# Kernel optimization log

Hardware: AMD Instinct MI355X
Metric: run time of the kernel (lower is better)

The kernel has to match this reference:

```python
import jax, jax.numpy as jnp
import numpy as np

B, S, D, H = 4, 1024, 512, 8
DH = D // H
NEG = -1e32


def setup_inputs() -> dict:
    key = jax.random.key(0)
    ks = jax.random.split(key, 8)
    w_scale = (6.0 / (D + D)) ** 0.5  # xavier_uniform bound scale (approx, gaussian draw)
    def nrm(i, shape, scale=1.0):
        return jax.random.normal(ks[i], shape, jnp.float32) * scale
    return {
        "q": nrm(0, (B, S, D)),
        "k": nrm(1, (B, S, D)),
        "v": nrm(2, (B, S, D)),
        # causal lower-triangular mask (attend to self and past)
        "mask": jnp.tril(jnp.ones((1, 1, S, S), jnp.int32)),
        "Wq": nrm(3, (D, D), w_scale), "bq": jnp.zeros((D,), jnp.float32),
        "Wk": nrm(4, (D, D), w_scale), "bk": jnp.zeros((D,), jnp.float32),
        "Wv": nrm(5, (D, D), w_scale), "bv": jnp.zeros((D,), jnp.float32),
        "Wo": nrm(6, (D, D), w_scale), "bo": jnp.zeros((D,), jnp.float32),
        "gammas": nrm(7, (H, 1, 1), 0.5),
    }


def reference(q, k, v, mask, Wq, bq, Wk, bk, Wv, bv, Wo, bo, gammas):
    maskf = mask.astype(jnp.float32)
    neg = mask == 0

    def proj(x, W, b):
        # nn.Linear: x @ W.T + b, then split heads -> [B,H,S,DH]
        return (x @ W.T + b).reshape(B, S, H, DH).transpose(0, 2, 1, 3)

    qh, kh, vh = proj(q, Wq, bq), proj(k, Wk, bk), proj(v, Wv, bv)
    scores = jnp.einsum('bhqd,bhkd->bhqk', qh, kh) / jnp.sqrt(jnp.float32(DH))

    pos = jnp.arange(S, dtype=jnp.float32)
    position_effect = jnp.abs(pos[None, :] - pos[:, None])  # [S,S] = |i - j|

    # no-grad branch: masked softmax -> cumulative / total attention mass
    sm = jax.nn.softmax(jnp.where(neg, NEG, scores), axis=-1) * maskf
    distcum = jnp.cumsum(sm, axis=-1)
    disttotal = jnp.sum(sm, axis=-1, keepdims=True)
    dist_scores = jnp.sqrt(jnp.maximum((disttotal - distcum) * position_effect, 0.0))
    dist_scores = jax.lax.stop_gradient(dist_scores)

    gamma = -jax.nn.softplus(gammas)[None]  # [1,H,1,1], learned decay rate
    total_effect = jnp.clip(jnp.exp(dist_scores * gamma), 1e-5, 1e5)

    attn = jax.nn.softmax(jnp.where(neg, NEG, scores * total_effect), axis=-1)
    attn = attn.at[:, :, 0, :].set(0.0)  # zero_pad=True: zero out first query row
    # dropout is identity at eval time

    out = jnp.einsum('bhqk,bhkd->bhqd', attn, vh)
    concat = out.transpose(0, 2, 1, 3).reshape(B, S, D)
    output = concat @ Wo.T + bo
    return output, attn
```

## Files before the change

kernel.cpp:

```cpp
#include <hip/hip_runtime.h>
#include <hip/hip_bf16.h>

typedef __attribute__((ext_vector_type(8))) _Float16 half8;
typedef __attribute__((ext_vector_type(4))) _Float16 half4v;
typedef __attribute__((ext_vector_type(4))) float f32x4;

#define MFMA16(a, b, c) __builtin_amdgcn_mfma_f32_16x16x32_f16((a), (b), (c), 0, 0, 0)

static constexpr int Bb = 4, Ss = 1024, Dd = 512, Hh = 8, DHh = 64;
static constexpr float LOG2E = 1.44269504f;
static constexpr float FNEG = -65504.f;

__device__ __forceinline__ half4v f2h4(float4 f) {
  half4v h;
  h[0] = (_Float16)f.x; h[1] = (_Float16)f.y;
  h[2] = (_Float16)f.z; h[3] = (_Float16)f.w;
  return h;
}

template<int MODE>
__global__ __launch_bounds__(256) void gemm_k(
    const void* A0v, const void* A1v, const float* Bm0, const float* Bm1,
    const float* bias0, const float* bias1, void* C0v, void* C1v,
    int M, int N, int K)
{
  __shared__ _Float16 As[128 * 72];
  __shared__ _Float16 Bs[64 * 72];

  const int tid = threadIdx.x;
  const int w = tid >> 6, l = tid & 63;
  const int wr = w >> 1, wc = w & 1;
  const int l4 = l >> 4, lm = l & 15;
  const int m0 = blockIdx.x * 128, n0 = blockIdx.y * 64;
  const int z = (MODE == 0) ? (int)blockIdx.z : 0;

  const float* Af = (const float*)(z ? A1v : A0v);
  const ushort* Ab = (const ushort*)A0v;
  const float* Bw = z ? Bm1 : Bm0;
  const float* bias = z ? bias1 : bias0;

  f32x4 zz = {0.f, 0.f, 0.f, 0.f};
  f32x4 acc[4][2];
#pragma unroll
  for (int i2 = 0; i2 < 4; ++i2)
#pragma unroll
    for (int j = 0; j < 2; ++j) acc[i2][j] = zz;

  for (int k0 = 0; k0 < K; k0 += 64) {
#pragma unroll
    for (int it = 0; it < 8; ++it) {
      int f4 = it * 256 + tid;
      int rowi = f4 >> 4, c4 = (f4 & 15) << 2;
      if constexpr (MODE == 1) {
        ushort4 u = *(const ushort4*)&Ab[(size_t)(m0 + rowi) * K + k0 + c4];
        *(ushort4*)&As[rowi * 72 + c4] = u;
      } else {
        float4 f = *(const float4*)&Af[(size_t)(m0 + rowi) * K + k0 + c4];
        *(half4v*)&As[rowi * 72 + c4] = f2h4(f);
      }
    }
#pragma unroll
    for (int it = 0; it < 4; ++it) {
      int f4 = it * 256 + tid;
      int rowi = f4 >> 4, c4 = (f4 & 15) << 2;
      float4 f = *(const float4*)&Bw[(size_t)(n0 + rowi) * K + k0 + c4];
      *(half4v*)&Bs[rowi * 72 + c4] = f2h4(f);
    }
    __syncthreads();
#pragma unroll
    for (int ks = 0; ks < 2; ++ks) {
      half8 a[4], b[2];
#pragma unroll
      for (int mf = 0; mf < 4; ++mf)
        a[mf] = *(const half8*)&As[(wr * 64 + mf * 16 + lm) * 72 + ks * 32 + l4 * 8];
#pragma unroll
      for (int nf = 0; nf < 2; ++nf)
        b[nf] = *(const half8*)&Bs[(wc * 32 + nf * 16 + lm) * 72 + ks * 32 + l4 * 8];
#pragma unroll
      for (int mf = 0; mf < 4; ++mf)
#pragma unroll
        for (int nf = 0; nf < 2; ++nf)
          acc[mf][nf] = MFMA16(a[mf], b[nf], acc[mf][nf]);
    }
    __syncthreads();
  }

  _Float16* Ch = (_Float16*)(z ? C1v : C0v);
  float* Cf = (float*)C0v;
#pragma unroll
  for (int mf = 0; mf < 4; ++mf) {
#pragma unroll
    for (int nf = 0; nf < 2; ++nf) {
      int row0 = m0 + wr * 64 + mf * 16 + l4 * 4;
      int col = n0 + wc * 32 + nf * 16 + lm;
      f32x4 vv = acc[mf][nf];
#pragma unroll
      for (int r = 0; r < 4; ++r) {
        int row = row0 + r;
        float val = vv[r];
        if constexpr (MODE == 0) {
          val += bias[col];
          int idx = (((row >> 10) * Hh + (col >> 6)) * Ss + (row & 1023)) * DHh + (col & 63);
          Ch[idx] = (_Float16)val;
        } else if constexpr (MODE == 2) {
          val += bias[row];
          int idx = (((col >> 10) * Hh + (row >> 6)) * DHh + (row & 63)) * Ss + (col & 1023);
          Ch[idx] = (_Float16)val;
        } else {
          val += bias[col];
          Cf[(size_t)row * N + col] = val;
        }
      }
    }
  }
}

__global__ __launch_bounds__(512, 4) void attn_k(
    const _Float16* __restrict__ qh, const _Float16* __restrict__ kh,
    const _Float16* __restrict__ vT, const float* __restrict__ gammas,
    float* __restrict__ attn_out, _Float16* __restrict__ concat)
{
  constexpr int TW = 1048;
  __shared__ __align__(16) float smemf[(32 * TW * 2 + 1024) / 4];
  _Float16* tile = (_Float16*)smemf;
  float* pmax = smemf + (32 * TW * 2) / 4;

  const int tid = threadIdx.x;
  const int w = tid >> 6, l = tid & 63;
  const int l4 = l >> 4, lm = l & 15;
  const int bh = blockIdx.y;
  const int b = bh >> 3, h = bh & 7;

  const float g = gammas[h];
  const float g2 = -log1pf(__expf(g)) * LOG2E;

  f32x4 zz = {0.f, 0.f, 0.f, 0.f};
  constexpr float SC2 = 0.125f * LOG2E;

  for (int half = 0; half < 2; ++half) {
    const int qr0 = half ? (Ss - 32 - blockIdx.x * 32) : (blockIdx.x * 32);
    const int nvalid = qr0 + 32;
    __syncthreads();

    const _Float16* Qp = qh + ((size_t)bh * Ss + qr0) * DHh;
    const _Float16* Kp = kh + (size_t)bh * Ss * DHh;

    {
      const int NF = nvalid >> 4;
      const int NFpad = ((nvalid + 63) & ~63) >> 4;
      half8 aq[2][2];
#pragma unroll
      for (int mf = 0; mf < 2; ++mf)
#pragma unroll
        for (int ks = 0; ks < 2; ++ks)
          aq[mf][ks] = *(const half8*)&Qp[(mf * 16 + lm) * DHh + ks * 32 + l4 * 8];

      float pmr[2][4];
#pragma unroll
      for (int mf = 0; mf < 2; ++mf)
#pragma unroll
        for (int r = 0; r < 4; ++r) pmr[mf][r] = -3.0e38f;

      for (int f = w; f < NFpad; f += 8) {
        f32x4 acc[2] = {zz, zz};
        const bool live = (f < NF);
        if (live) {
#pragma unroll
          for (int ks = 0; ks < 2; ++ks) {
            half8 bb = *(const half8*)&Kp[(size_t)(f * 16 + lm) * DHh + ks * 32 + l4 * 8];
            acc[0] = MFMA16(aq[0][ks], bb, acc[0]);
            acc[1] = MFMA16(aq[1][ks], bb, acc[1]);
          }
        }
        const int colc = f * 16 + lm;
#pragma unroll
        for (int mf = 0; mf < 2; ++mf)
#pragma unroll
          for (int r = 0; r < 4; ++r) {
            const int rg = mf * 16 + l4 * 4 + r;
            float val = (live && colc <= qr0 + rg) ? acc[mf][r] * SC2 : FNEG;
            tile[rg * TW + colc] = (_Float16)val;
            pmr[mf][r] = fmaxf(pmr[mf][r], val);
          }
      }
#pragma unroll
      for (int d = 1; d < 16; d <<= 1)
#pragma unroll
        for (int mf = 0; mf < 2; ++mf)
#pragma unroll
          for (int r = 0; r < 4; ++r)
            pmr[mf][r] = fmaxf(pmr[mf][r], __shfl_xor(pmr[mf][r], d, 16));
      if (lm == 0) {
#pragma unroll
        for (int mf = 0; mf < 2; ++mf)
#pragma unroll
          for (int r = 0; r < 4; ++r)
            pmax[(mf * 16 + l4 * 4 + r) * 8 + w] = pmr[mf][r];
      }
    }
    __syncthreads();

    {
      const int r = tid >> 4, t = tid & 15;
      const int i = qr0 + r;
      const int L = i + 1;
      const int nch = (L + 63) >> 6;
      _Float16* row = tile + r * TW;

      float mx = (t < 8) ? pmax[r * 8 + t] : -3.0e38f;
#pragma unroll
      for (int d = 8; d; d >>= 1) mx = fmaxf(mx, __shfl_xor(mx, d, 16));

      float T = 0.f;
      for (int c = 0; c < nch; ++c) {
        half4v s4 = *(const half4v*)&row[(c << 6) + (t << 2)];
#pragma unroll
        for (int j = 0; j < 4; ++j) T += exp2f((float)s4[j] - mx);
      }
#pragma unroll
      for (int d = 8; d; d >>= 1) T += __shfl_xor(T, d, 16);
      const float invT = 1.f / T;

      float carry = 0.f, m2 = -3.0e38f;
      for (int c = 0; c < nch; ++c) {
        const int col = (c << 6) + (t << 2);
        half4v s4 = *(const half4v*)&row[col];
        float s[4], e[4];
#pragma unroll
        for (int j = 0; j < 4; ++j) {
          s[j] = (float)s4[j];
          e[j] = exp2f(s[j] - mx);
        }
        const float lsum = (e[0] + e[1]) + (e[2] + e[3]);
        float sc = lsum;
#pragma unroll
        for (int d = 1; d < 16; d <<= 1) {
          float o = __shfl_up(sc, d, 16);
          if (t >= d) sc += o;
        }
        float run = carry + (sc - lsum);
        carry += __shfl(sc, 15, 16);
        const float dj = (float)(i - col);
        half4v o4;
#pragma unroll
        for (int j = 0; j < 4; ++j) {
          run += e[j];
          float prod = fmaxf((T - run) * invT * (dj - (float)j), 0.f);
          float dist = sqrtf(prod);
          float eff = fmaxf(exp2f(g2 * dist), 1e-5f);
          float l2 = s[j] * eff;
          o4[j] = (_Float16)l2;
          m2 = fmaxf(m2, l2);
        }
        *(half4v*)&row[col] = o4;
      }
#pragma unroll
      for (int d = 8; d; d >>= 1) m2 = fmaxf(m2, __shfl_xor(m2, d, 16));

      float Z2 = 0.f;
      for (int c = 0; c < nch; ++c) {
        const int col = (c << 6) + (t << 2);
        half4v l4v = *(const half4v*)&row[col];
        half4v u4;
#pragma unroll
        for (int j = 0; j < 4; ++j) {
          float u = exp2f((float)l4v[j] - m2);
          Z2 += u;
          u4[j] = (_Float16)u;
        }
        *(half4v*)&row[col] = u4;
      }
#pragma unroll
      for (int d = 8; d; d >>= 1) Z2 += __shfl_xor(Z2, d, 16);
      const float invZ2 = 1.f / Z2;

      const bool zrow = (i == 0);
      float* arow = attn_out + ((size_t)bh * Ss + i) * Ss;
      for (int c = 0; c < Ss / 64; ++c) {
        const int col = (c << 6) + (t << 2);
        float4 pv = {0.f, 0.f, 0.f, 0.f};
        float* pp = (float*)&pv;
        if (c < nch) {
          if (!zrow) {
            half4v u4 = *(const half4v*)&row[col];
#pragma unroll
            for (int j = 0; j < 4; ++j) pp[j] = (float)u4[j] * invZ2;
          }
          half4v p4;
#pragma unroll
          for (int j = 0; j < 4; ++j) p4[j] = (_Float16)pp[j];
          *(half4v*)&row[col] = p4;
        }
        *(float4*)&arow[col] = pv;
      }
    }
    __syncthreads();

    f32x4 acc2[2][4];
#pragma unroll
    for (int mf = 0; mf < 2; ++mf)
#pragma unroll
      for (int nf = 0; nf < 4; ++nf) acc2[mf][nf] = zz;
    {
      const int NC = nvalid >> 5;
      const _Float16* Vp = vT + (size_t)bh * DHh * Ss;
      for (int c = w; c < NC; c += 8) {
        const int kb = c << 5;
        half8 pa[2];
#pragma unroll
        for (int mf = 0; mf < 2; ++mf)
          pa[mf] = *(const half8*)&tile[(mf * 16 + lm) * TW + kb + l4 * 8];
#pragma unroll
        for (int nf = 0; nf < 4; ++nf) {
          half8 bb = *(const half8*)&Vp[(size_t)(nf * 16 + lm) * Ss + kb + l4 * 8];
          acc2[0][nf] = MFMA16(pa[0], bb, acc2[0][nf]);
          acc2[1][nf] = MFMA16(pa[1], bb, acc2[1][nf]);
        }
      }
    }
    __syncthreads();
    float* pps = smemf;
#pragma unroll
    for (int mf = 0; mf < 2; ++mf)
#pragma unroll
      for (int nf = 0; nf < 4; ++nf)
#pragma unroll
        for (int r = 0; r < 4; ++r)
          pps[w * 2048 + (mf * 16 + l4 * 4 + r) * 64 + nf * 16 + lm] = acc2[mf][nf][r];
    __syncthreads();
    for (int idx = tid; idx < 2048; idx += 512) {
      int mr = idx >> 6, nc = idx & 63;
      float ssum = 0.f;
#pragma unroll
      for (int ww = 0; ww < 8; ++ww) ssum += pps[ww * 2048 + idx];
      concat[((size_t)(b * Ss + qr0 + mr)) * Dd + h * DHh + nc] = (_Float16)ssum;
    }
  }
}

extern "C" void kernel_launch(void* const* d_in, const int* in_sizes, int n_in,
                              void* d_out, int out_size, void* d_ws, size_t ws_size,
                              hipStream_t stream) {
  const float* q  = (const float*)d_in[0];
  const float* k  = (const float*)d_in[1];
  const float* v  = (const float*)d_in[2];
  const float* Wq = (const float*)d_in[4];
  const float* bq = (const float*)d_in[5];
  const float* Wk = (const float*)d_in[6];
  const float* bk = (const float*)d_in[7];
  const float* Wv = (const float*)d_in[8];
  const float* bv = (const float*)d_in[9];
  const float* Wo = (const float*)d_in[10];
  const float* bo = (const float*)d_in[11];
  const float* gm = (const float*)d_in[12];

  _Float16* qhb = (_Float16*)d_ws;
  _Float16* khb = qhb + 2097152;
  _Float16* vT  = khb + 2097152;
  _Float16* cc  = vT  + 2097152;

  float* out  = (float*)d_out;
  float* attn = out + (size_t)Bb * Ss * Dd;

  gemm_k<0><<<dim3(32, 8, 2), 256, 0, stream>>>(q, k, Wq, Wk, bq, bk, qhb, khb,
                                                4096, 512, 512);
  gemm_k<2><<<dim3(4, 64, 1), 256, 0, stream>>>(Wv, nullptr, v, nullptr, bv, nullptr,
                                                vT, nullptr, 512, 4096, 512);
  attn_k<<<dim3(16, 32), 512, 0, stream>>>(qhb, khb, vT, gm, attn, cc);
  gemm_k<1><<<dim3(32, 8, 1), 256, 0, stream>>>(cc, nullptr, Wo, nullptr, bo, nullptr,
                                                out, nullptr, 4096, 512, 512);
}
```

Before: 105.9 us.

## Stream attention in 512-column panels with online softmax stats and recomputed QK

Replaces the full-row score tile held in shared memory with 512-column panels. The first pass computes online max and sum statistics, and QK^T is recomputed for a Z2 pass and again for the output pass. The PV product is accumulated per panel, one 16x16 fragment per wave, which removes the cross-wave reduction through shared memory. Shared memory per block shrinks, allowing more blocks per CU (launch bounds 6) and one query tile per block over a doubled grid. The cost is running QK^T and the exp/sqrt effect math three times instead of once, plus a fixed max shift (max(mx,0)) for the second softmax instead of the true row max.

```diff
diff --git a/kernel.cpp b/kernel.cpp
--- a/kernel.cpp
+++ b/kernel.cpp
@@ -115,226 +115,262 @@
   }
 }
 
-__global__ __launch_bounds__(512, 4) void attn_k(
+__global__ __launch_bounds__(512, 6) void attn_k(
     const _Float16* __restrict__ qh, const _Float16* __restrict__ kh,
     const _Float16* __restrict__ vT, const float* __restrict__ gammas,
     float* __restrict__ attn_out, _Float16* __restrict__ concat)
 {
-  constexpr int TW = 1048;
-  __shared__ __align__(16) float smemf[(32 * TW * 2 + 1024) / 4];
-  _Float16* tile = (_Float16*)smemf;
-  float* pmax = smemf + (32 * TW * 2) / 4;
+  constexpr int TW = 528;
+  __shared__ __align__(16) _Float16 tile[32 * TW];
+  __shared__ float pm[256], pt[256];
 
   const int tid = threadIdx.x;
   const int w = tid >> 6, l = tid & 63;
   const int l4 = l >> 4, lm = l & 15;
   const int bh = blockIdx.y;
   const int b = bh >> 3, h = bh & 7;
+  const int qr0 = Ss - 32 - blockIdx.x * 32;
+  const int nvalid = qr0 + 32;
+  const int NF = nvalid >> 4;
+  const int Npan = (nvalid + 511) >> 9;
 
   const float g = gammas[h];
   const float g2 = -log1pf(__expf(g)) * LOG2E;
+  constexpr float SC2 = 0.125f * LOG2E;
+
+  const _Float16* Qp = qh + ((size_t)bh * Ss + qr0) * DHh;
+  const _Float16* Kp = kh + (size_t)bh * Ss * DHh;
+  const _Float16* Vp = vT + (size_t)bh * DHh * Ss;
 
   f32x4 zz = {0.f, 0.f, 0.f, 0.f};
-  constexpr float SC2 = 0.125f * LOG2E;
-
-  for (int half = 0; half < 2; ++half) {
-    const int qr0 = half ? (Ss - 32 - blockIdx.x * 32) : (blockIdx.x * 32);
-    const int nvalid = qr0 + 32;
-    __syncthreads();
-
-    const _Float16* Qp = qh + ((size_t)bh * Ss + qr0) * DHh;
-    const _Float16* Kp = kh + (size_t)bh * Ss * DHh;
-
-    {
-      const int NF = nvalid >> 4;
-      const int NFpad = ((nvalid + 63) & ~63) >> 4;
-      half8 aq[2][2];
+
+  half8 aq[2][2];
+#pragma unroll
+  for (int mf = 0; mf < 2; ++mf)
+#pragma unroll
+    for (int ks = 0; ks < 2; ++ks)
+      aq[mf][ks] = *(const half8*)&Qp[(mf * 16 + lm) * DHh + ks * 32 + l4 * 8];
+
+  {
+    float m_[2][4], t_[2][4];
+#pragma unroll
+    for (int mf = 0; mf < 2; ++mf)
+#pragma unroll
+      for (int r = 0; r < 4; ++r) { m_[mf][r] = -3.0e38f; t_[mf][r] = 0.f; }
+
+    for (int f = w; f < NF; f += 8) {
+      f32x4 acc[2] = {zz, zz};
+      const int colc = f * 16 + lm;
+#pragma unroll
+      for (int ks = 0; ks < 2; ++ks) {
+        half8 bb = *(const half8*)&Kp[(size_t)colc * DHh + ks * 32 + l4 * 8];
+        acc[0] = MFMA16(aq[0][ks], bb, acc[0]);
+        acc[1] = MFMA16(aq[1][ks], bb, acc[1]);
+      }
 #pragma unroll
       for (int mf = 0; mf < 2; ++mf)
 #pragma unroll
-        for (int ks = 0; ks < 2; ++ks)
-          aq[mf][ks] = *(const half8*)&Qp[(mf * 16 + lm) * DHh + ks * 32 + l4 * 8];
-
-      float pmr[2][4];
+        for (int r = 0; r < 4; ++r) {
+          const int rg = mf * 16 + l4 * 4 + r;
+          const bool vld = colc <= qr0 + rg;
+          float s = (float)(_Float16)(acc[mf][r] * SC2);
+          float sv = vld ? s : -3.0e38f;
+          float mN = fmaxf(m_[mf][r], sv);
+          t_[mf][r] = t_[mf][r] * exp2f(m_[mf][r] - mN) + (vld ? exp2f(sv - mN) : 0.f);
+          m_[mf][r] = mN;
+        }
+    }
+#pragma unroll
+    for (int d = 1; d < 16; d <<= 1)
 #pragma unroll
       for (int mf = 0; mf < 2; ++mf)
 #pragma unroll
-        for (int r = 0; r < 4; ++r) pmr[mf][r] = -3.0e38f;
-
-      for (int f = w; f < NFpad; f += 8) {
+        for (int r = 0; r < 4; ++r) {
+          float mo = __shfl_xor(m_[mf][r], d, 16);
+          float to = __shfl_xor(t_[mf][r], d, 16);
+          float mN = fmaxf(m_[mf][r], mo);
+          t_[mf][r] = t_[mf][r] * exp2f(m_[mf][r] - mN) + to * exp2f(mo - mN);
+          m_[mf][r] = mN;
+        }
+    if (lm == 0) {
+#pragma unroll
+      for (int mf = 0; mf < 2; ++mf)
+#pragma unroll
+        for (int r = 0; r < 4; ++r) {
+          const int rg = mf * 16 + l4 * 4 + r;
+          pm[rg * 8 + w] = m_[mf][r];
+          pt[rg * 8 + w] = t_[mf][r];
+        }
+    }
+  }
+  __syncthreads();
+
+  const int rr_ = tid >> 4, t16 = tid & 15;
+  const int i_ = qr0 + rr_;
+
+  float mx = -3.0e38f, T = 0.f;
+#pragma unroll
+  for (int ww = 0; ww < 8; ++ww) {
+    float mo = pm[rr_ * 8 + ww], to = pt[rr_ * 8 + ww];
+    float mN = fmaxf(mx, mo);
+    T = T * exp2f(mx - mN) + to * exp2f(mo - mN);
+    mx = mN;
+  }
+  const float invT = 1.f / T;
+  const float Msh = fmaxf(mx, 0.f);
+
+  float Z2 = 0.f;
+  {
+    float carry = 0.f;
+    for (int p = 0; p < Npan; ++p) {
+#pragma unroll
+      for (int j = 0; j < 4; ++j) {
+        const int floc = w + j * 8;
+        const int f = p * 32 + floc;
+        const int colc = f * 16 + lm;
         f32x4 acc[2] = {zz, zz};
-        const bool live = (f < NF);
-        if (live) {
+        if (f < NF) {
 #pragma unroll
           for (int ks = 0; ks < 2; ++ks) {
-            half8 bb = *(const half8*)&Kp[(size_t)(f * 16 + lm) * DHh + ks * 32 + l4 * 8];
+            half8 bb = *(const half8*)&Kp[(size_t)colc * DHh + ks * 32 + l4 * 8];
             acc[0] = MFMA16(aq[0][ks], bb, acc[0]);
             acc[1] = MFMA16(aq[1][ks], bb, acc[1]);
           }
         }
-        const int colc = f * 16 + lm;
+        const int lcol = floc * 16 + lm;
 #pragma unroll
         for (int mf = 0; mf < 2; ++mf)
 #pragma unroll
           for (int r = 0; r < 4; ++r) {
             const int rg = mf * 16 + l4 * 4 + r;
-            float val = (live && colc <= qr0 + rg) ? acc[mf][r] * SC2 : FNEG;
-            tile[rg * TW + colc] = (_Float16)val;
-            pmr[mf][r] = fmaxf(pmr[mf][r], val);
+            float val = (f < NF && colc <= qr0 + rg) ? acc[mf][r] * SC2 : FNEG;
+            tile[rg * TW + lcol] = (_Float16)val;
           }
       }
-#pragma unroll
-      for (int d = 1; d < 16; d <<= 1)
-#pragma unroll
-        for (int mf = 0; mf < 2; ++mf)
-#pragma unroll
-          for (int r = 0; r < 4; ++r)
-            pmr[mf][r] = fmaxf(pmr[mf][r], __shfl_xor(pmr[mf][r], d, 16));
-      if (lm == 0) {
-#pragma unroll
-        for (int mf = 0; mf < 2; ++mf)
-#pragma unroll
-          for (int r = 0; r < 4; ++r)
-            pmax[(mf * 16 + l4 * 4 + r) * 8 + w] = pmr[mf][r];
-      }
-    }
-    __syncthreads();
-
-    {
-      const int r = tid >> 4, t = tid & 15;
-      const int i = qr0 + r;
-      const int L = i + 1;
-      const int nch = (L + 63) >> 6;
-      _Float16* row = tile + r * TW;
-
-      float mx = (t < 8) ? pmax[r * 8 + t] : -3.0e38f;
-#pragma unroll
-      for (int d = 8; d; d >>= 1) mx = fmaxf(mx, __shfl_xor(mx, d, 16));
-
-      float T = 0.f;
-      for (int c = 0; c < nch; ++c) {
-        half4v s4 = *(const half4v*)&row[(c << 6) + (t << 2)];
-#pragma unroll
-        for (int j = 0; j < 4; ++j) T += exp2f((float)s4[j] - mx);
-      }
-#pragma unroll
-      for (int d = 8; d; d >>= 1) T += __shfl_xor(T, d, 16);
-      const float invT = 1.f / T;
-
-      float carry = 0.f, m2 = -3.0e38f;
-      for (int c = 0; c < nch; ++c) {
-        const int col = (c << 6) + (t << 2);
-        half4v s4 = *(const half4v*)&row[col];
+      __syncthreads();
+      for (int cl = 0; cl < 8; ++cl) {
+        const int cb = p * 512 + cl * 64;
+        if (cb > i_) break;
+        half4v s4 = *(const half4v*)&tile[rr_ * TW + cl * 64 + (t16 << 2)];
         float s[4], e[4];
 #pragma unroll
-        for (int j = 0; j < 4; ++j) {
-          s[j] = (float)s4[j];
-          e[j] = exp2f(s[j] - mx);
-        }
+        for (int j = 0; j < 4; ++j) { s[j] = (float)s4[j]; e[j] = exp2f(s[j] - mx); }
         const float lsum = (e[0] + e[1]) + (e[2] + e[3]);
         float sc = lsum;
 #pragma unroll
         for (int d = 1; d < 16; d <<= 1) {
           float o = __shfl_up(sc, d, 16);
-          if (t >= d) sc += o;
+          if (t16 >= d) sc += o;
         }
         float run = carry + (sc - lsum);
         carry += __shfl(sc, 15, 16);
-        const float dj = (float)(i - col);
-        half4v o4;
+        const float dj = (float)(i_ - (cb + (t16 << 2)));
 #pragma unroll
         for (int j = 0; j < 4; ++j) {
           run += e[j];
           float prod = fmaxf((T - run) * invT * (dj - (float)j), 0.f);
-          float dist = sqrtf(prod);
-          float eff = fmaxf(exp2f(g2 * dist), 1e-5f);
-          float l2 = s[j] * eff;
-          o4[j] = (_Float16)l2;
-          m2 = fmaxf(m2, l2);
-        }
-        *(half4v*)&row[col] = o4;
-      }
-#pragma unroll
-      for (int d = 8; d; d >>= 1) m2 = fmaxf(m2, __shfl_xor(m2, d, 16));
-
-      float Z2 = 0.f;
-      for (int c = 0; c < nch; ++c) {
-        const int col = (c << 6) + (t << 2);
-        half4v l4v = *(const half4v*)&row[col];
-        half4v u4;
+          float eff = fmaxf(exp2f(g2 * sqrtf(prod)), 1e-5f);
+          Z2 += exp2f(s[j] * eff - Msh);
+        }
+      }
+      __syncthreads();
+    }
+  }
+#pragma unroll
+  for (int d = 1; d < 16; d <<= 1) Z2 += __shfl_xor(Z2, d, 16);
+  const float invZ2 = 1.f / Z2;
+
+  f32x4 accO = zz;
+  const int mfw = w >> 2, nfw = w & 3;
+  {
+    float carry = 0.f;
+    const bool zrow = (i_ == 0);
+    float* arow = attn_out + ((size_t)bh * Ss + i_) * Ss;
+    const float4 z4 = {0.f, 0.f, 0.f, 0.f};
+    const half4v hz4 = {(_Float16)0.f, (_Float16)0.f, (_Float16)0.f, (_Float16)0.f};
+
+    for (int p = 0; p < Npan; ++p) {
+#pragma unroll
+      for (int j = 0; j < 4; ++j) {
+        const int floc = w + j * 8;
+        const int f = p * 32 + floc;
+        const int colc = f * 16 + lm;
+        f32x4 acc[2] = {zz, zz};
+        if (f < NF) {
+#pragma unroll
+          for (int ks = 0; ks < 2; ++ks) {
+            half8 bb = *(const half8*)&Kp[(size_t)colc * DHh + ks * 32 + l4 * 8];
+            acc[0] = MFMA16(aq[0][ks], bb, acc[0]);
+            acc[1] = MFMA16(aq[1][ks], bb, acc[1]);
+          }
+        }
+        const int lcol = floc * 16 + lm;
+#pragma unroll
+        for (int mf = 0; mf < 2; ++mf)
+#pragma unroll
+          for (int r = 0; r < 4; ++r) {
+            const int rg = mf * 16 + l4 * 4 + r;
+            float val = (f < NF && colc <= qr0 + rg) ? acc[mf][r] * SC2 : FNEG;
+            tile[rg * TW + lcol] = (_Float16)val;
+          }
+      }
+      __syncthreads();
+      for (int cl = 0; cl < 8; ++cl) {
+        const int cb = p * 512 + cl * 64;
+        const int lofs = rr_ * TW + cl * 64 + (t16 << 2);
+        if (cb > i_) {
+          *(half4v*)&tile[lofs] = hz4;
+          *(float4*)&arow[cb + (t16 << 2)] = z4;
+          continue;
+        }
+        half4v s4 = *(const half4v*)&tile[lofs];
+        float s[4], e[4];
+#pragma unroll
+        for (int j = 0; j < 4; ++j) { s[j] = (float)s4[j]; e[j] = exp2f(s[j] - mx); }
+        const float lsum = (e[0] + e[1]) + (e[2] + e[3]);
+        float sc = lsum;
+#pragma unroll
+        for (int d = 1; d < 16; d <<= 1) {
+          float o = __shfl_up(sc, d, 16);
+          if (t16 >= d) sc += o;
+        }
+        float run = carry + (sc - lsum);
+        carry += __shfl(sc, 15, 16);
+        const float dj = (float)(i_ - (cb + (t16 << 2)));
+        float4 pv = z4;
+        float* pp = (float*)&pv;
+        half4v p4;
 #pragma unroll
         for (int j = 0; j < 4; ++j) {
-          float u = exp2f((float)l4v[j] - m2);
-          Z2 += u;
-          u4[j] = (_Float16)u;
-        }
-        *(half4v*)&row[col] = u4;
-      }
-#pragma unroll
-      for (int d = 8; d; d >>= 1) Z2 += __shfl_xor(Z2, d, 16);
-      const float invZ2 = 1.f / Z2;
-
-      const bool zrow = (i == 0);
-      float* arow = attn_out + ((size_t)bh * Ss + i) * Ss;
-      for (int c = 0; c < Ss / 64; ++c) {
-        const int col = (c << 6) + (t << 2);
-        float4 pv = {0.f, 0.f, 0.f, 0.f};
-        float* pp = (float*)&pv;
-        if (c < nch) {
-          if (!zrow) {
-            half4v u4 = *(const half4v*)&row[col];
-#pragma unroll
-            for (int j = 0; j < 4; ++j) pp[j] = (float)u4[j] * invZ2;
-          }
-          half4v p4;
-#pragma unroll
-          for (int j = 0; j < 4; ++j) p4[j] = (_Float16)pp[j];
-          *(half4v*)&row[col] = p4;
-        }
-        *(float4*)&arow[col] = pv;
-      }
-    }
-    __syncthreads();
-
-    f32x4 acc2[2][4];
-#pragma unroll
-    for (int mf = 0; mf < 2; ++mf)
-#pragma unroll
-      for (int nf = 0; nf < 4; ++nf) acc2[mf][nf] = zz;
-    {
-      const int NC = nvalid >> 5;
-      const _Float16* Vp = vT + (size_t)bh * DHh * Ss;
-      for (int c = w; c < NC; c += 8) {
-        const int kb = c << 5;
-        half8 pa[2];
-#pragma unroll
-        for (int mf = 0; mf < 2; ++mf)
-          pa[mf] = *(const half8*)&tile[(mf * 16 + lm) * TW + kb + l4 * 8];
-#pragma unroll
-        for (int nf = 0; nf < 4; ++nf) {
-          half8 bb = *(const half8*)&Vp[(size_t)(nf * 16 + lm) * Ss + kb + l4 * 8];
-          acc2[0][nf] = MFMA16(pa[0], bb, acc2[0][nf]);
-          acc2[1][nf] = MFMA16(pa[1], bb, acc2[1][nf]);
-        }
-      }
-    }
-    __syncthreads();
-    float* pps = smemf;
-#pragma unroll
-    for (int mf = 0; mf < 2; ++mf)
-#pragma unroll
-      for (int nf = 0; nf < 4; ++nf)
-#pragma unroll
-        for (int r = 0; r < 4; ++r)
-          pps[w * 2048 + (mf * 16 + l4 * 4 + r) * 64 + nf * 16 + lm] = acc2[mf][nf][r];
-    __syncthreads();
-    for (int idx = tid; idx < 2048; idx += 512) {
-      int mr = idx >> 6, nc = idx & 63;
-      float ssum = 0.f;
-#pragma unroll
-      for (int ww = 0; ww < 8; ++ww) ssum += pps[ww * 2048 + idx];
-      concat[((size_t)(b * Ss + qr0 + mr)) * Dd + h * DHh + nc] = (_Float16)ssum;
-    }
+          run += e[j];
+          float prod = fmaxf((T - run) * invT * (dj - (float)j), 0.f);
+          float eff = fmaxf(exp2f(g2 * sqrtf(prod)), 1e-5f);
+          float u = exp2f(s[j] * eff - Msh);
+          float P = zrow ? 0.f : u * invZ2;
+          pp[j] = P;
+          p4[j] = (_Float16)P;
+        }
+        *(half4v*)&tile[lofs] = p4;
+        *(float4*)&arow[cb + (t16 << 2)] = pv;
+      }
+      __syncthreads();
+      const int ksmax = min(16, (nvalid - p * 512 + 31) >> 5);
+      for (int ks = 0; ks < ksmax; ++ks) {
+        const int kb = ks * 32;
+        half8 pa = *(const half8*)&tile[(mfw * 16 + lm) * TW + kb + l4 * 8];
+        half8 bb = *(const half8*)&Vp[(size_t)(nfw * 16 + lm) * Ss + p * 512 + kb + l4 * 8];
+        accO = MFMA16(pa, bb, accO);
+      }
+      __syncthreads();
+    }
+    for (int c = Npan * 8; c < 16; ++c)
+      *(float4*)&arow[c * 64 + (t16 << 2)] = z4;
+  }
+
+#pragma unroll
+  for (int r = 0; r < 4; ++r) {
+    const int row = qr0 + mfw * 16 + l4 * 4 + r;
+    concat[((size_t)(b * Ss + row)) * Dd + h * DHh + nfw * 16 + lm] = (_Float16)accO[r];
   }
 }
 
@@ -366,7 +402,7 @@
                                                 4096, 512, 512);
   gemm_k<2><<<dim3(4, 64, 1), 256, 0, stream>>>(Wv, nullptr, v, nullptr, bv, nullptr,
                                                 vT, nullptr, 512, 4096, 512);
-  attn_k<<<dim3(16, 32), 512, 0, stream>>>(qhb, khb, vT, gm, attn, cc);
+  attn_k<<<dim3(32, 32), 512, 0, stream>>>(qhb, khb, vT, gm, attn, cc);
   gemm_k<1><<<dim3(32, 8, 1), 256, 0, stream>>>(cc, nullptr, Wo, nullptr, bo, nullptr,
                                                 out, nullptr, 4096, 512, 512);
 }
```

Result: slower. 243.3 us (+129.7%).

## Fuse online softmax denominator into QK pass and merge decay/exp passes

Applied to the files above, without the earlier changes.

Computes the running max and exp-sum per row online during the QK^T MFMA pass, so the separate pass that recomputed the first softmax denominator is dropped. The decayed-logit pass and the second exp pass are merged by using a fixed shift max(rowmax, 0) instead of a recomputed second max. The per-wave partial max and sum now live in a padding region of the tile row, which removes the separate pmax array. The fixed shift relies on decay factors at most 1 so that exp2 of the scaled logit stays bounded. It also adds two exp2 per element to the QK loop.

```diff
diff --git a/kernel.cpp b/kernel.cpp
--- a/kernel.cpp
+++ b/kernel.cpp
@@ -120,10 +120,8 @@
     const _Float16* __restrict__ vT, const float* __restrict__ gammas,
     float* __restrict__ attn_out, _Float16* __restrict__ concat)
 {
-  constexpr int TW = 1048;
-  __shared__ __align__(16) float smemf[(32 * TW * 2 + 1024) / 4];
-  _Float16* tile = (_Float16*)smemf;
-  float* pmax = smemf + (32 * TW * 2) / 4;
+  constexpr int TW = 1064;
+  __shared__ __align__(16) _Float16 tile[32 * TW];
 
   const int tid = threadIdx.x;
   const int w = tid >> 6, l = tid & 63;
@@ -133,9 +131,9 @@
 
   const float g = gammas[h];
   const float g2 = -log1pf(__expf(g)) * LOG2E;
+  constexpr float SC2 = 0.125f * LOG2E;
 
   f32x4 zz = {0.f, 0.f, 0.f, 0.f};
-  constexpr float SC2 = 0.125f * LOG2E;
 
   for (int half = 0; half < 2; ++half) {
     const int qr0 = half ? (Ss - 32 - blockIdx.x * 32) : (blockIdx.x * 32);
@@ -155,11 +153,11 @@
         for (int ks = 0; ks < 2; ++ks)
           aq[mf][ks] = *(const half8*)&Qp[(mf * 16 + lm) * DHh + ks * 32 + l4 * 8];
 
-      float pmr[2][4];
+      float m_[2][4], t_[2][4];
 #pragma unroll
       for (int mf = 0; mf < 2; ++mf)
 #pragma unroll
-        for (int r = 0; r < 4; ++r) pmr[mf][r] = -3.0e38f;
+        for (int r = 0; r < 4; ++r) { m_[mf][r] = -3.0e38f; t_[mf][r] = 0.f; }
 
       for (int f = w; f < NFpad; f += 8) {
         f32x4 acc[2] = {zz, zz};
@@ -179,8 +177,12 @@
           for (int r = 0; r < 4; ++r) {
             const int rg = mf * 16 + l4 * 4 + r;
             float val = (live && colc <= qr0 + rg) ? acc[mf][r] * SC2 : FNEG;
-            tile[rg * TW + colc] = (_Float16)val;
-            pmr[mf][r] = fmaxf(pmr[mf][r], val);
+            _Float16 vh = (_Float16)val;
+            tile[rg * TW + colc] = vh;
+            val = (float)vh;
+            float mN = fmaxf(m_[mf][r], val);
+            t_[mf][r] = t_[mf][r] * exp2f(m_[mf][r] - mN) + exp2f(val - mN);
+            m_[mf][r] = mN;
           }
       }
 #pragma unroll
@@ -188,42 +190,48 @@
 #pragma unroll
         for (int mf = 0; mf < 2; ++mf)
 #pragma unroll
-          for (int r = 0; r < 4; ++r)
-            pmr[mf][r] = fmaxf(pmr[mf][r], __shfl_xor(pmr[mf][r], d, 16));
+          for (int r = 0; r < 4; ++r) {
+            float mo = __shfl_xor(m_[mf][r], d, 16);
+            float to = __shfl_xor(t_[mf][r], d, 16);
+            float mN = fmaxf(m_[mf][r], mo);
+            t_[mf][r] = t_[mf][r] * exp2f(m_[mf][r] - mN) + to * exp2f(mo - mN);
+            m_[mf][r] = mN;
+          }
       if (lm == 0) {
 #pragma unroll
         for (int mf = 0; mf < 2; ++mf)
 #pragma unroll
-          for (int r = 0; r < 4; ++r)
-            pmax[(mf * 16 + l4 * 4 + r) * 8 + w] = pmr[mf][r];
+          for (int r = 0; r < 4; ++r) {
+            const int rg = mf * 16 + l4 * 4 + r;
+            float* sp = (float*)&tile[rg * TW + 1024];
+            sp[w] = m_[mf][r];
+            sp[8 + w] = t_[mf][r];
+          }
       }
     }
     __syncthreads();
 
     {
-      const int r = tid >> 4, t = tid & 15;
-      const int i = qr0 + r;
-      const int L = i + 1;
-      const int nch = (L + 63) >> 6;
-      _Float16* row = tile + r * TW;
-
-      float mx = (t < 8) ? pmax[r * 8 + t] : -3.0e38f;
-#pragma unroll
-      for (int d = 8; d; d >>= 1) mx = fmaxf(mx, __shfl_xor(mx, d, 16));
-
-      float T = 0.f;
+      const int rr = tid >> 4, t16 = tid & 15;
+      const int i = qr0 + rr;
+      const int nch = (i >> 6) + 1;
+      _Float16* row = tile + rr * TW;
+      const float* sp = (const float*)&row[1024];
+
+      float mx = -3.0e38f, T = 0.f;
+#pragma unroll
+      for (int ww = 0; ww < 8; ++ww) {
+        float mo = sp[ww], to = sp[8 + ww];
+        float mN = fmaxf(mx, mo);
+        T = T * exp2f(mx - mN) + to * exp2f(mo - mN);
+        mx = mN;
+      }
+      const float invT = 1.f / T;
+      const float Msh = fmaxf(mx, 0.f);
+
+      float carry = 0.f, Z2 = 0.f;
       for (int c = 0; c < nch; ++c) {
-        half4v s4 = *(const half4v*)&row[(c << 6) + (t << 2)];
-#pragma unroll
-        for (int j = 0; j < 4; ++j) T += exp2f((float)s4[j] - mx);
-      }
-#pragma unroll
-      for (int d = 8; d; d >>= 1) T += __shfl_xor(T, d, 16);
-      const float invT = 1.f / T;
-
-      float carry = 0.f, m2 = -3.0e38f;
-      for (int c = 0; c < nch; ++c) {
-        const int col = (c << 6) + (t << 2);
+        const int col = (c << 6) + (t16 << 2);
         half4v s4 = *(const half4v*)&row[col];
         float s[4], e[4];
 #pragma unroll
@@ -236,37 +244,20 @@
 #pragma unroll
         for (int d = 1; d < 16; d <<= 1) {
           float o = __shfl_up(sc, d, 16);
-          if (t >= d) sc += o;
+          if (t16 >= d) sc += o;
         }
         float run = carry + (sc - lsum);
         carry += __shfl(sc, 15, 16);
         const float dj = (float)(i - col);
-        half4v o4;
+        half4v u4;
 #pragma unroll
         for (int j = 0; j < 4; ++j) {
           run += e[j];
           float prod = fmaxf((T - run) * invT * (dj - (float)j), 0.f);
-          float dist = sqrtf(prod);
-          float eff = fmaxf(exp2f(g2 * dist), 1e-5f);
-          float l2 = s[j] * eff;
-          o4[j] = (_Float16)l2;
-          m2 = fmaxf(m2, l2);
-        }
-        *(half4v*)&row[col] = o4;
-      }
-#pragma unroll
-      for (int d = 8; d; d >>= 1) m2 = fmaxf(m2, __shfl_xor(m2, d, 16));
-
-      float Z2 = 0.f;
-      for (int c = 0; c < nch; ++c) {
-        const int col = (c << 6) + (t << 2);
-        half4v l4v = *(const half4v*)&row[col];
-        half4v u4;
-#pragma unroll
-        for (int j = 0; j < 4; ++j) {
-          float u = exp2f((float)l4v[j] - m2);
-          Z2 += u;
-          u4[j] = (_Float16)u;
+          float eff = fmaxf(exp2f(g2 * sqrtf(prod)), 1e-5f);
+          float uu = exp2f(s[j] * eff - Msh);
+          Z2 += uu;
+          u4[j] = (_Float16)uu;
         }
         *(half4v*)&row[col] = u4;
       }
@@ -277,7 +268,7 @@
       const bool zrow = (i == 0);
       float* arow = attn_out + ((size_t)bh * Ss + i) * Ss;
       for (int c = 0; c < Ss / 64; ++c) {
-        const int col = (c << 6) + (t << 2);
+        const int col = (c << 6) + (t16 << 2);
         float4 pv = {0.f, 0.f, 0.f, 0.f};
         float* pp = (float*)&pv;
         if (c < nch) {
@@ -319,7 +310,7 @@
       }
     }
     __syncthreads();
-    float* pps = smemf;
+    float* pps = (float*)tile;
 #pragma unroll
     for (int mf = 0; mf < 2; ++mf)
 #pragma unroll
```

Result: slower. 114.4 us (+8.0%).
